# Kernel optimization log

Measured on AMD Instinct MI355X. Metric: run time of the kernel, lower is better.

Reference implementation:

```python
import jax, jax.numpy as jnp
import numpy as np


def setup_inputs() -> dict:
    key = jax.random.key(0)
    k1, k2, k3, k4 = jax.random.split(key, 4)
    in_f, out_f, rank, tokens = 4096, 4096, 256, 8192
    bound = 1.0 / np.sqrt(in_f)
    x = jax.random.normal(k1, (tokens, in_f), dtype=jnp.float32)
    U = jax.random.uniform(k2, (out_f, rank), dtype=jnp.float32, minval=-bound, maxval=bound)
    V = jax.random.uniform(k3, (rank, in_f), dtype=jnp.float32, minval=-bound, maxval=bound)
    bias = jax.random.uniform(k4, (out_f,), dtype=jnp.float32, minval=-bound, maxval=bound)
    return {"x": x, "U": U, "V": V, "bias": bias}


def reference(x, U, V, bias):
    # Faithful to original: materialize W = U @ V, then F.linear(x, W, bias) = x @ W.T + bias
    W = U @ V                      # [out, in]
    return x @ W.T + bias          # [tokens, out]
```

## Files before the change

kernel.cpp:

```cpp
#include <hip/hip_runtime.h>
#include <stdint.h>

#define TOKENS 8192
#define INF    4096
#define OUTF   4096
#define RANK   256

typedef __attribute__((ext_vector_type(8))) short bf16x8;
typedef __attribute__((ext_vector_type(4))) float f32x4;

__device__ __forceinline__ unsigned short f2bf(float f) {
    union { float f; unsigned int u; } v; v.f = f;
    unsigned int r = v.u + 0x7FFFu + ((v.u >> 16) & 1u);
    return (unsigned short)(r >> 16);
}

__device__ __forceinline__ void gl_lds16(const void* g, void* l) {
    __builtin_amdgcn_global_load_lds(
        (const __attribute__((address_space(1))) unsigned int*)g,
        (__attribute__((address_space(3))) unsigned int*)l, 16, 0, 0);
}

__global__ void cvt4(const float4* __restrict__ in, ushort4* __restrict__ out) {
    int i = blockIdx.x * blockDim.x + threadIdx.x;
    float4 v = in[i];
    ushort4 o;
    o.x = f2bf(v.x); o.y = f2bf(v.y); o.z = f2bf(v.z); o.w = f2bf(v.w);
    out[i] = o;
}

#define G1_BM 32
#define G1_BN 128
#define G1_BK 128
#define A1_STR 136

__global__ __launch_bounds__(512) void gemm1(const float* __restrict__ x,
                                             const unsigned short* __restrict__ Vb,
                                             unsigned short* __restrict__ T) {
    __shared__ __align__(16) unsigned short Axlds[G1_BM * A1_STR];
    __shared__ __align__(16) unsigned short Bvlds[G1_BN * G1_BK];

    const int tid  = threadIdx.x;
    const int lane = tid & 63;
    const int wid  = tid >> 6;
    const int m0   = blockIdx.y * G1_BM;
    const int n0   = blockIdx.x * G1_BN;
    const int l15  = lane & 15;
    const int quad = lane >> 4;

    const int arow = tid >> 4;
    const int aseg = tid & 15;
    const float* xa = x + (size_t)(m0 + arow) * INF + aseg * 8;
    unsigned short* alds_w = &Axlds[arow * A1_STR + aseg * 8];

    const int b_lrow = lane >> 4;
    const int b_pos  = lane & 15;

    f32x4 acc[2];
    acc[0] = (f32x4){0.f, 0.f, 0.f, 0.f};
    acc[1] = (f32x4){0.f, 0.f, 0.f, 0.f};

    for (int kk = 0; kk < INF; kk += G1_BK) {
        #pragma unroll
        for (int j = 0; j < 4; ++j) {
            int r0  = j * 32 + wid * 4;
            int row = r0 + b_lrow;
            int cf  = b_pos ^ (row & 7);
            gl_lds16(Vb + (size_t)(n0 + row) * INF + kk + cf * 8,
                     &Bvlds[r0 * G1_BK]);
        }
        float4 va = *(const float4*)(xa + kk);
        float4 vb = *(const float4*)(xa + kk + 4);
        {
            union { bf16x8 v; unsigned short s[8]; } pk;
            pk.s[0] = f2bf(va.x); pk.s[1] = f2bf(va.y);
            pk.s[2] = f2bf(va.z); pk.s[3] = f2bf(va.w);
            pk.s[4] = f2bf(vb.x); pk.s[5] = f2bf(vb.y);
            pk.s[6] = f2bf(vb.z); pk.s[7] = f2bf(vb.w);
            *(bf16x8*)alds_w = pk.v;
        }
        __syncthreads();
        #pragma unroll
        for (int ks = 0; ks < 4; ++ks) {
            int rr = wid * 16 + l15;
            int p  = (ks * 4 + quad) ^ (rr & 7);
            bf16x8 aV = *(const bf16x8*)&Bvlds[rr * G1_BK + p * 8];
            #pragma unroll
            for (int mt = 0; mt < 2; ++mt) {
                int tr = mt * 16 + l15;
                bf16x8 bx = *(const bf16x8*)&Axlds[tr * A1_STR + ks * 32 + quad * 8];
                acc[mt] = __builtin_amdgcn_mfma_f32_16x16x32_bf16(aV, bx, acc[mt], 0, 0, 0);
            }
        }
        __syncthreads();
    }
    #pragma unroll
    for (int mt = 0; mt < 2; ++mt) {
        int m      = m0 + mt * 16 + l15;
        int n_base = n0 + wid * 16 + quad * 4;
        ushort4 o;
        o.x = f2bf(acc[mt][0]); o.y = f2bf(acc[mt][1]);
        o.z = f2bf(acc[mt][2]); o.w = f2bf(acc[mt][3]);
        *(ushort4*)&T[(size_t)m * RANK + n_base] = o;
    }
}

#define G2_BM 128
#define G2_BN 128
#define G2_BK 64

__global__ __launch_bounds__(256) void gemm2(const unsigned short* __restrict__ Tb,
                                             const unsigned short* __restrict__ Ub,
                                             const float* __restrict__ bias,
                                             float* __restrict__ out) {
    __shared__ __align__(16) unsigned short Tlds[G2_BM * G2_BK];
    __shared__ __align__(16) unsigned short Ulds[G2_BN * G2_BK];

    const int tid  = threadIdx.x;
    const int lane = tid & 63;
    const int wid  = tid >> 6;
    const int wy   = wid >> 1, wx = wid & 1;
    const int m0   = blockIdx.y * G2_BM;
    const int n0   = blockIdx.x * G2_BN;
    const int l15  = lane & 15, quad = lane >> 4;
    const int lrow = lane >> 3;
    const int cf   = (lane & 7) ^ lrow;

    f32x4 acc[4][4];
    #pragma unroll
    for (int i = 0; i < 4; i++)
        #pragma unroll
        for (int j = 0; j < 4; j++) acc[i][j] = (f32x4){0.f, 0.f, 0.f, 0.f};

    for (int kk = 0; kk < RANK; kk += G2_BK) {
        #pragma unroll
        for (int j = 0; j < 4; ++j) {
            int r0 = wid * 32 + j * 8;
            gl_lds16(Tb + (size_t)(m0 + r0 + lrow) * RANK + kk + cf * 8,
                     &Tlds[r0 * G2_BK]);
            gl_lds16(Ub + (size_t)(n0 + r0 + lrow) * RANK + kk + cf * 8,
                     &Ulds[r0 * G2_BK]);
        }
        __syncthreads();
        #pragma unroll
        for (int ks = 0; ks < 2; ++ks) {
            bf16x8 aU[4], bT[4];
            #pragma unroll
            for (int t = 0; t < 4; ++t) {
                int ur = wx * 64 + t * 16 + l15;
                int up = (ks * 4 + quad) ^ (ur & 7);
                aU[t] = *(const bf16x8*)&Ulds[ur * G2_BK + up * 8];
                int tr = wy * 64 + t * 16 + l15;
                int tp = (ks * 4 + quad) ^ (tr & 7);
                bT[t] = *(const bf16x8*)&Tlds[tr * G2_BK + tp * 8];
            }
            #pragma unroll
            for (int nt = 0; nt < 4; ++nt)
                #pragma unroll
                for (int mt = 0; mt < 4; ++mt)
                    acc[nt][mt] = __builtin_amdgcn_mfma_f32_16x16x32_bf16(
                        aU[nt], bT[mt], acc[nt][mt], 0, 0, 0);
        }
        __syncthreads();
    }
    float4 bv[4];
    #pragma unroll
    for (int nt = 0; nt < 4; ++nt)
        bv[nt] = *(const float4*)&bias[n0 + wx * 64 + nt * 16 + quad * 4];
    #pragma unroll
    for (int nt = 0; nt < 4; ++nt) {
        int n_base = n0 + wx * 64 + nt * 16 + quad * 4;
        #pragma unroll
        for (int mt = 0; mt < 4; ++mt) {
            int m = m0 + wy * 64 + mt * 16 + l15;
            float4 v;
            v.x = acc[nt][mt][0] + bv[nt].x;
            v.y = acc[nt][mt][1] + bv[nt].y;
            v.z = acc[nt][mt][2] + bv[nt].z;
            v.w = acc[nt][mt][3] + bv[nt].w;
            *(float4*)&out[(size_t)m * OUTF + n_base] = v;
        }
    }
}

extern "C" void kernel_launch(void* const* d_in, const int* in_sizes, int n_in,
                              void* d_out, int out_size, void* d_ws, size_t ws_size,
                              hipStream_t stream) {
    const float* x    = (const float*)d_in[0];
    const float* U    = (const float*)d_in[1];
    const float* V    = (const float*)d_in[2];
    const float* bias = (const float*)d_in[3];
    float* out = (float*)d_out;

    unsigned short* Vb = (unsigned short*)d_ws;
    unsigned short* Ub = Vb + (size_t)RANK * INF;
    unsigned short* Tb = Ub + (size_t)OUTF * RANK;

    cvt4<<<(RANK * INF / 4) / 256, 256, 0, stream>>>((const float4*)V, (ushort4*)Vb);
    cvt4<<<(OUTF * RANK / 4) / 256, 256, 0, stream>>>((const float4*)U, (ushort4*)Ub);
    gemm1<<<dim3(RANK / G1_BN, TOKENS / G1_BM), 512, 0, stream>>>(x, Vb, Tb);
    gemm2<<<dim3(OUTF / G2_BN, TOKENS / G2_BM), 256, 0, stream>>>(Tb, Ub, bias, out);
}
```

Before: 294.0 us.

## Widen gemm1 to full rank per block and double-buffer both GEMMs

gemm1 now has each block cover all 256 rank columns for 32 tokens. This halves the grid and means x is read and converted once, not twice. V fragments are loaded straight from global memory into registers and prefetched, while the x tile is double-buffered in LDS with a single barrier per stage. gemm2 double-buffers its T/U LDS tiles so the next k-slice loads while the current one computes, and it hoists the bias load. The risks are extra register pressure, uncoalesced per-lane V reads from global memory that are not shared through LDS, and gemm1 launching only 256 blocks.

```diff
diff --git a/kernel.cpp b/kernel.cpp
--- a/kernel.cpp
+++ b/kernel.cpp
@@ -30,91 +30,135 @@
 }
 
 #define G1_BM 32
-#define G1_BN 128
 #define G1_BK 128
 #define A1_STR 136
+
+__device__ __forceinline__ void g1_loadV(bf16x8 (&V)[2][4],
+                                         const unsigned short* vr0,
+                                         const unsigned short* vr1,
+                                         int kk, int quad) {
+    #pragma unroll
+    for (int ks = 0; ks < 4; ++ks) {
+        V[0][ks] = *(const bf16x8*)(vr0 + kk + ks * 32 + quad * 8);
+        V[1][ks] = *(const bf16x8*)(vr1 + kk + ks * 32 + quad * 8);
+    }
+}
+
+__device__ __forceinline__ void g1_compute(f32x4 (&acc)[2][2],
+                                           const bf16x8 (&V)[2][4],
+                                           const unsigned short* ax,
+                                           int l15, int quad) {
+    #pragma unroll
+    for (int ks = 0; ks < 4; ++ks) {
+        bf16x8 b0 = *(const bf16x8*)(ax + l15 * A1_STR + ks * 32 + quad * 8);
+        bf16x8 b1 = *(const bf16x8*)(ax + (16 + l15) * A1_STR + ks * 32 + quad * 8);
+        acc[0][0] = __builtin_amdgcn_mfma_f32_16x16x32_bf16(V[0][ks], b0, acc[0][0], 0, 0, 0);
+        acc[0][1] = __builtin_amdgcn_mfma_f32_16x16x32_bf16(V[0][ks], b1, acc[0][1], 0, 0, 0);
+        acc[1][0] = __builtin_amdgcn_mfma_f32_16x16x32_bf16(V[1][ks], b0, acc[1][0], 0, 0, 0);
+        acc[1][1] = __builtin_amdgcn_mfma_f32_16x16x32_bf16(V[1][ks], b1, acc[1][1], 0, 0, 0);
+    }
+}
+
+__device__ __forceinline__ void g1_pack(float4 a, float4 b, unsigned short* dst) {
+    union { bf16x8 v; unsigned short s[8]; } pk;
+    pk.s[0] = f2bf(a.x); pk.s[1] = f2bf(a.y);
+    pk.s[2] = f2bf(a.z); pk.s[3] = f2bf(a.w);
+    pk.s[4] = f2bf(b.x); pk.s[5] = f2bf(b.y);
+    pk.s[6] = f2bf(b.z); pk.s[7] = f2bf(b.w);
+    *(bf16x8*)dst = pk.v;
+}
 
 __global__ __launch_bounds__(512) void gemm1(const float* __restrict__ x,
                                              const unsigned short* __restrict__ Vb,
                                              unsigned short* __restrict__ T) {
-    __shared__ __align__(16) unsigned short Axlds[G1_BM * A1_STR];
-    __shared__ __align__(16) unsigned short Bvlds[G1_BN * G1_BK];
+    __shared__ __align__(16) unsigned short Ax[2][G1_BM * A1_STR];
 
     const int tid  = threadIdx.x;
     const int lane = tid & 63;
     const int wid  = tid >> 6;
-    const int m0   = blockIdx.y * G1_BM;
-    const int n0   = blockIdx.x * G1_BN;
+    const int m0   = blockIdx.x * G1_BM;
     const int l15  = lane & 15;
     const int quad = lane >> 4;
 
     const int arow = tid >> 4;
     const int aseg = tid & 15;
-    const float* xa = x + (size_t)(m0 + arow) * INF + aseg * 8;
-    unsigned short* alds_w = &Axlds[arow * A1_STR + aseg * 8];
-
-    const int b_lrow = lane >> 4;
-    const int b_pos  = lane & 15;
-
-    f32x4 acc[2];
-    acc[0] = (f32x4){0.f, 0.f, 0.f, 0.f};
-    acc[1] = (f32x4){0.f, 0.f, 0.f, 0.f};
-
-    for (int kk = 0; kk < INF; kk += G1_BK) {
-        #pragma unroll
-        for (int j = 0; j < 4; ++j) {
-            int r0  = j * 32 + wid * 4;
-            int row = r0 + b_lrow;
-            int cf  = b_pos ^ (row & 7);
-            gl_lds16(Vb + (size_t)(n0 + row) * INF + kk + cf * 8,
-                     &Bvlds[r0 * G1_BK]);
+    const float* xp = x + (size_t)(m0 + arow) * INF + aseg * 8;
+    unsigned short* aw0 = &Ax[0][arow * A1_STR + aseg * 8];
+    unsigned short* aw1 = &Ax[1][arow * A1_STR + aseg * 8];
+
+    const unsigned short* vr0 = Vb + (size_t)(wid * 32 + l15) * INF;
+    const unsigned short* vr1 = vr0 + (size_t)16 * INF;
+
+    f32x4 acc[2][2];
+    #pragma unroll
+    for (int i = 0; i < 2; ++i)
+        #pragma unroll
+        for (int j = 0; j < 2; ++j) acc[i][j] = (f32x4){0.f, 0.f, 0.f, 0.f};
+
+    bf16x8 VA[2][4], VB[2][4];
+
+    float4 xr0 = *(const float4*)(xp);
+    float4 xr1 = *(const float4*)(xp + 4);
+    g1_pack(xr0, xr1, aw0);
+    g1_loadV(VA, vr0, vr1, 0, quad);
+
+    for (int kt = 0; kt < 32; kt += 2) {
+        const int k1 = (kt + 1) * G1_BK;
+        const int k2 = (kt + 2 < 32 ? kt + 2 : 31) * G1_BK;
+
+        __syncthreads();
+        xr0 = *(const float4*)(xp + k1);
+        xr1 = *(const float4*)(xp + k1 + 4);
+        g1_loadV(VB, vr0, vr1, k1, quad);
+        g1_compute(acc, VA, &Ax[0][0], l15, quad);
+        g1_pack(xr0, xr1, aw1);
+
+        __syncthreads();
+        xr0 = *(const float4*)(xp + k2);
+        xr1 = *(const float4*)(xp + k2 + 4);
+        g1_loadV(VA, vr0, vr1, k2, quad);
+        g1_compute(acc, VB, &Ax[1][0], l15, quad);
+        g1_pack(xr0, xr1, aw0);
+    }
+
+    #pragma unroll
+    for (int mv = 0; mv < 2; ++mv) {
+        #pragma unroll
+        for (int mx = 0; mx < 2; ++mx) {
+            int m = m0 + mx * 16 + l15;
+            int n = wid * 32 + mv * 16 + quad * 4;
+            ushort4 o;
+            o.x = f2bf(acc[mv][mx][0]); o.y = f2bf(acc[mv][mx][1]);
+            o.z = f2bf(acc[mv][mx][2]); o.w = f2bf(acc[mv][mx][3]);
+            *(ushort4*)&T[(size_t)m * RANK + n] = o;
         }
-        float4 va = *(const float4*)(xa + kk);
-        float4 vb = *(const float4*)(xa + kk + 4);
-        {
-            union { bf16x8 v; unsigned short s[8]; } pk;
-            pk.s[0] = f2bf(va.x); pk.s[1] = f2bf(va.y);
-            pk.s[2] = f2bf(va.z); pk.s[3] = f2bf(va.w);
-            pk.s[4] = f2bf(vb.x); pk.s[5] = f2bf(vb.y);
-            pk.s[6] = f2bf(vb.z); pk.s[7] = f2bf(vb.w);
-            *(bf16x8*)alds_w = pk.v;
-        }
-        __syncthreads();
-        #pragma unroll
-        for (int ks = 0; ks < 4; ++ks) {
-            int rr = wid * 16 + l15;
-            int p  = (ks * 4 + quad) ^ (rr & 7);
-            bf16x8 aV = *(const bf16x8*)&Bvlds[rr * G1_BK + p * 8];
-            #pragma unroll
-            for (int mt = 0; mt < 2; ++mt) {
-                int tr = mt * 16 + l15;
-                bf16x8 bx = *(const bf16x8*)&Axlds[tr * A1_STR + ks * 32 + quad * 8];
-                acc[mt] = __builtin_amdgcn_mfma_f32_16x16x32_bf16(aV, bx, acc[mt], 0, 0, 0);
-            }
-        }
-        __syncthreads();
-    }
-    #pragma unroll
-    for (int mt = 0; mt < 2; ++mt) {
-        int m      = m0 + mt * 16 + l15;
-        int n_base = n0 + wid * 16 + quad * 4;
-        ushort4 o;
-        o.x = f2bf(acc[mt][0]); o.y = f2bf(acc[mt][1]);
-        o.z = f2bf(acc[mt][2]); o.w = f2bf(acc[mt][3]);
-        *(ushort4*)&T[(size_t)m * RANK + n_base] = o;
     }
 }
 
 #define G2_BM 128
 #define G2_BN 128
 #define G2_BK 64
+
+__device__ __forceinline__ void g2_stage(unsigned short (&Tl)[2][G2_BM * G2_BK],
+                                         unsigned short (&Ul)[2][G2_BN * G2_BK],
+                                         int b, int kk,
+                                         const unsigned short* Tb,
+                                         const unsigned short* Ub,
+                                         int m0, int n0, int wid, int lrow, int cf) {
+    #pragma unroll
+    for (int j = 0; j < 4; ++j) {
+        int r0 = wid * 32 + j * 8;
+        gl_lds16(Tb + (size_t)(m0 + r0 + lrow) * RANK + kk + cf * 8, &Tl[b][r0 * G2_BK]);
+        gl_lds16(Ub + (size_t)(n0 + r0 + lrow) * RANK + kk + cf * 8, &Ul[b][r0 * G2_BK]);
+    }
+}
 
 __global__ __launch_bounds__(256) void gemm2(const unsigned short* __restrict__ Tb,
                                              const unsigned short* __restrict__ Ub,
                                              const float* __restrict__ bias,
                                              float* __restrict__ out) {
-    __shared__ __align__(16) unsigned short Tlds[G2_BM * G2_BK];
-    __shared__ __align__(16) unsigned short Ulds[G2_BN * G2_BK];
+    __shared__ __align__(16) unsigned short Tlds[2][G2_BM * G2_BK];
+    __shared__ __align__(16) unsigned short Ulds[2][G2_BN * G2_BK];
 
     const int tid  = threadIdx.x;
     const int lane = tid & 63;
@@ -132,27 +176,31 @@
         #pragma unroll
         for (int j = 0; j < 4; j++) acc[i][j] = (f32x4){0.f, 0.f, 0.f, 0.f};
 
-    for (int kk = 0; kk < RANK; kk += G2_BK) {
-        #pragma unroll
-        for (int j = 0; j < 4; ++j) {
-            int r0 = wid * 32 + j * 8;
-            gl_lds16(Tb + (size_t)(m0 + r0 + lrow) * RANK + kk + cf * 8,
-                     &Tlds[r0 * G2_BK]);
-            gl_lds16(Ub + (size_t)(n0 + r0 + lrow) * RANK + kk + cf * 8,
-                     &Ulds[r0 * G2_BK]);
-        }
+    float4 bv[4];
+    #pragma unroll
+    for (int nt = 0; nt < 4; ++nt)
+        bv[nt] = *(const float4*)&bias[n0 + wx * 64 + nt * 16 + quad * 4];
+
+    g2_stage(Tlds, Ulds, 0, 0, Tb, Ub, m0, n0, wid, lrow, cf);
+
+    #pragma unroll
+    for (int t = 0; t < 4; ++t) {
         __syncthreads();
+        if (t < 3)
+            g2_stage(Tlds, Ulds, (t + 1) & 1, (t + 1) * G2_BK,
+                     Tb, Ub, m0, n0, wid, lrow, cf);
+        const int b = t & 1;
         #pragma unroll
         for (int ks = 0; ks < 2; ++ks) {
             bf16x8 aU[4], bT[4];
             #pragma unroll
-            for (int t = 0; t < 4; ++t) {
-                int ur = wx * 64 + t * 16 + l15;
+            for (int tt = 0; tt < 4; ++tt) {
+                int ur = wx * 64 + tt * 16 + l15;
                 int up = (ks * 4 + quad) ^ (ur & 7);
-                aU[t] = *(const bf16x8*)&Ulds[ur * G2_BK + up * 8];
-                int tr = wy * 64 + t * 16 + l15;
+                aU[tt] = *(const bf16x8*)&Ulds[b][ur * G2_BK + up * 8];
+                int tr = wy * 64 + tt * 16 + l15;
                 int tp = (ks * 4 + quad) ^ (tr & 7);
-                bT[t] = *(const bf16x8*)&Tlds[tr * G2_BK + tp * 8];
+                bT[tt] = *(const bf16x8*)&Tlds[b][tr * G2_BK + tp * 8];
             }
             #pragma unroll
             for (int nt = 0; nt < 4; ++nt)
@@ -161,12 +209,8 @@
                     acc[nt][mt] = __builtin_amdgcn_mfma_f32_16x16x32_bf16(
                         aU[nt], bT[mt], acc[nt][mt], 0, 0, 0);
         }
-        __syncthreads();
-    }
-    float4 bv[4];
-    #pragma unroll
-    for (int nt = 0; nt < 4; ++nt)
-        bv[nt] = *(const float4*)&bias[n0 + wx * 64 + nt * 16 + quad * 4];
+    }
+
     #pragma unroll
     for (int nt = 0; nt < 4; ++nt) {
         int n_base = n0 + wx * 64 + nt * 16 + quad * 4;
@@ -198,6 +242,6 @@
 
     cvt4<<<(RANK * INF / 4) / 256, 256, 0, stream>>>((const float4*)V, (ushort4*)Vb);
     cvt4<<<(OUTF * RANK / 4) / 256, 256, 0, stream>>>((const float4*)U, (ushort4*)Ub);
-    gemm1<<<dim3(RANK / G1_BN, TOKENS / G1_BM), 512, 0, stream>>>(x, Vb, Tb);
+    gemm1<<<TOKENS / G1_BM, 512, 0, stream>>>(x, Vb, Tb);
     gemm2<<<dim3(OUTF / G2_BN, TOKENS / G2_BM), 256, 0, stream>>>(Tb, Ub, bias, out);
 }
```

Result: slower. 300.3 us (+2.1%).
